# Kernel optimization log

Measured on AMD Instinct MI355X. Metric: run time of the kernel, lower is better.

The kernel has to match this reference:

```python
import jax, jax.numpy as jnp
import numpy as np

D_MODEL = 1024
N_HEADS = 16
N_KV_HEADS = 4
HEAD_DIM = D_MODEL // N_HEADS  # 64
N_REP = N_HEADS // N_KV_HEADS  # 4
THETA = 10000.0
LOGIT_CAP = 30.0
EPS = 1e-6
SCALE = HEAD_DIM ** -0.5


def rmsnorm(x, w):
    return x * jax.lax.rsqrt(jnp.mean(x * x, axis=-1, keepdims=True) + EPS) * w


def rope_tables(seq_len, dtype):
    inv_freq = 1.0 / (THETA ** (jnp.arange(0, HEAD_DIM, 2, dtype=jnp.float32) / HEAD_DIM))
    t = jnp.arange(seq_len, dtype=jnp.float32)
    freqs = jnp.outer(t, inv_freq)                      # [S, hd/2]
    emb = jnp.concatenate([freqs, freqs], axis=-1)      # [S, hd]
    return jnp.cos(emb).astype(dtype), jnp.sin(emb).astype(dtype)


def rotate_half(x):
    x1, x2 = jnp.split(x, 2, axis=-1)
    return jnp.concatenate([-x2, x1], axis=-1)


def apply_rope(x, cos, sin):
    # x: [B, H, S, hd]; cos/sin: [S, hd] broadcast over (B, H)
    return x * cos + rotate_half(x) * sin


def setup_inputs() -> dict:
    key = jax.random.key(0)
    ks = jax.random.split(key, 7)
    B, S = 4, 2048
    w = 0.02
    return {
        "x": jax.random.normal(ks[0], (B, S, D_MODEL), dtype=jnp.float32),
        "Wq": jax.random.normal(ks[1], (N_HEADS * HEAD_DIM, D_MODEL), dtype=jnp.float32) * w,
        "Wk": jax.random.normal(ks[2], (N_KV_HEADS * HEAD_DIM, D_MODEL), dtype=jnp.float32) * w,
        "Wv": jax.random.normal(ks[3], (N_KV_HEADS * HEAD_DIM, D_MODEL), dtype=jnp.float32) * w,
        "Wo": jax.random.normal(ks[4], (D_MODEL, N_HEADS * HEAD_DIM), dtype=jnp.float32) * w,
        "q_norm_w": jnp.ones((HEAD_DIM,), dtype=jnp.float32),
        "k_norm_w": jnp.ones((HEAD_DIM,), dtype=jnp.float32),
    }


def reference(x, Wq, Wk, Wv, Wo, q_norm_w, k_norm_w):
    B, S, _ = x.shape
    # projections (nn.Linear: y = x @ W^T)
    q = (x @ Wq.T).reshape(B, S, N_HEADS, HEAD_DIM).transpose(0, 2, 1, 3)      # [B,H,S,d]
    k = (x @ Wk.T).reshape(B, S, N_KV_HEADS, HEAD_DIM).transpose(0, 2, 1, 3)   # [B,Hkv,S,d]
    v = (x @ Wv.T).reshape(B, S, N_KV_HEADS, HEAD_DIM).transpose(0, 2, 1, 3)
    # QK-RMSNorm
    q = rmsnorm(q, q_norm_w)
    k = rmsnorm(k, k_norm_w)
    # RoPE
    cos, sin = rope_tables(S, x.dtype)
    q = apply_rope(q, cos, sin)
    k = apply_rope(k, cos, sin)
    # GQA expand (repeat_interleave over head dim)
    k_exp = jnp.repeat(k, N_REP, axis=1)  # [B,H,S,d]
    v_exp = jnp.repeat(v, N_REP, axis=1)
    # soft-capped attention (training path)
    scores = jnp.einsum('bhqd,bhkd->bhqk', q, k_exp) * SCALE
    scores = LOGIT_CAP * jnp.tanh(scores / LOGIT_CAP)
    causal = jnp.triu(jnp.ones((S, S), dtype=bool), k=1)  # kv_len - seq_len + 1 = 1
    scores = jnp.where(causal, -jnp.inf, scores)
    attn = jax.nn.softmax(scores, axis=-1)
    out = jnp.einsum('bhqk,bhkd->bhqd', attn, v_exp)
    out = out.transpose(0, 2, 1, 3).reshape(B, S, N_HEADS * HEAD_DIM)
    return out @ Wo.T
```

## Files before the change

### kernel.cpp

```cpp
#include <hip/hip_runtime.h>
#include <hip/hip_bf16.h>
#include <math.h>
#include <stdint.h>

#define D_MODEL 1024
#define NHEADS  16
#define NKV     4
#define HD      64
#define SEQ     2048
#define BATCH   4
#define MTOK    (BATCH*SEQ)
#define NQKV    (D_MODEL + 2*NKV*HD)
#define ASCALE  0.125f
#define CAP     30.0f

using f32x4  = __attribute__((ext_vector_type(4))) float;
using f32x2  = __attribute__((ext_vector_type(2))) float;
using bf16x8 = __attribute__((ext_vector_type(8))) short;

__device__ __forceinline__ unsigned short f2bf(float f) {
  union { float f; unsigned u; } v; v.f = f;
  unsigned u = v.u + 0x7fffu + ((v.u >> 16) & 1u);
  return (unsigned short)(u >> 16);
}
__device__ __forceinline__ unsigned short f2bf_hup(float f) {
  union { float f; unsigned u; } v; v.f = f;
  return (unsigned short)((v.u + 0x8000u) >> 16);
}
__device__ __forceinline__ float fexp2(float x) {
  return __builtin_amdgcn_exp2f(x);
}
__device__ __forceinline__ void async_copy16(void* lds, const void* g) {
  __builtin_amdgcn_global_load_lds(
      (const __attribute__((address_space(1))) unsigned int*)(uintptr_t)g,
      (__attribute__((address_space(3))) unsigned int*)(uintptr_t)lds, 16, 0, 0);
}

__global__ __launch_bounds__(256) void cvt_all(
    const float* __restrict__ x, const float* __restrict__ wq,
    const float* __restrict__ wk, const float* __restrict__ wv,
    const float* __restrict__ wo,
    unsigned short* __restrict__ xb, unsigned short* __restrict__ wqkv,
    unsigned short* __restrict__ wob) {
  const long i = (long)(blockIdx.x * 256 + threadIdx.x) * 4;
  const float* src; unsigned short* dst; long off;
  if (i < 8388608L)      { src = x;  dst = xb;             off = i; }
  else if (i < 9437184L) { src = wq; dst = wqkv;           off = i - 8388608L; }
  else if (i < 9699328L) { src = wk; dst = wqkv + 1048576; off = i - 9437184L; }
  else if (i < 9961472L) { src = wv; dst = wqkv + 1310720; off = i - 9699328L; }
  else                   { src = wo; dst = wob;            off = i - 9961472L; }
  float4 v = *(const float4*)(src + off);
  ushort4 o; o.x = f2bf(v.x); o.y = f2bf(v.y); o.z = f2bf(v.z); o.w = f2bf(v.w);
  *(ushort4*)(dst + off) = o;
}

__global__ __launch_bounds__(256) void gemm_qkv(
    const unsigned short* __restrict__ A, const unsigned short* __restrict__ B,
    const float* __restrict__ qw, const float* __restrict__ kw,
    unsigned short* __restrict__ Qn, unsigned short* __restrict__ Kn,
    unsigned short* __restrict__ Vt) {
  __shared__ __align__(16) unsigned short As[128 * 32];
  __shared__ __align__(16) unsigned short Bs[128 * 32];
  const int t = threadIdx.x;
  const int w = t >> 6, l = t & 63;
  const int mb = blockIdx.x, nb = blockIdx.y;
  const int wm = w & 1, wn = w >> 1;
  const int quad = l >> 4, ln = l & 15;
  const int K = D_MODEL;
  f32x4 acc[4][4] = {};
  const unsigned short* Ag = A + (size_t)(mb * 128 + w * 32) * K;
  const unsigned short* Bg = B + (size_t)(nb * 128 + w * 32) * K;
  char* Asw = (char*)As + w * 2048;
  char* Bsw = (char*)Bs + w * 2048;
  const int lrow = l >> 2, lcol = (l & 3) * 8;

  for (int kb = 0; kb < K; kb += 32) {
    async_copy16(Asw + l * 16,        Ag + (size_t)lrow * K + kb + lcol);
    async_copy16(Asw + 1024 + l * 16, Ag + (size_t)(16 + lrow) * K + kb + lcol);
    async_copy16(Bsw + l * 16,        Bg + (size_t)lrow * K + kb + lcol);
    async_copy16(Bsw + 1024 + l * 16, Bg + (size_t)(16 + lrow) * K + kb + lcol);
    __syncthreads();
    bf16x8 af[4], bfr[4];
#pragma unroll
    for (int mt = 0; mt < 4; ++mt)
      af[mt] = *(const bf16x8*)(As + (wm * 64 + mt * 16 + ln) * 32 + quad * 8);
#pragma unroll
    for (int nt = 0; nt < 4; ++nt)
      bfr[nt] = *(const bf16x8*)(Bs + (wn * 64 + nt * 16 + ln) * 32 + quad * 8);
#pragma unroll
    for (int mt = 0; mt < 4; ++mt)
#pragma unroll
      for (int nt = 0; nt < 4; ++nt)
        acc[mt][nt] = __builtin_amdgcn_mfma_f32_16x16x32_bf16(af[mt], bfr[nt], acc[mt][nt], 0, 0, 0);
    __syncthreads();
  }

  const int hs = nb * 2 + wn;
  const int bB = mb >> 4;
  const int sBase = ((mb & 15) * 128) + wm * 64;

  if (hs < 20) {
    const float* wgt = (hs < 16) ? qw : kw;
    float wv_[4];
#pragma unroll
    for (int nt = 0; nt < 4; ++nt) wv_[nt] = wgt[nt * 16 + ln];
    const float f0 = __expf(-(float)ln * 0.2878231366f);
    const float f1 = f0 * 0.01f;
    unsigned short* dst = (hs < 16)
        ? Qn + (size_t)(bB * 16 + hs) * SEQ * 64
        : Kn + (size_t)(bB * 4 + (hs - 16)) * SEQ * 64;
#pragma unroll
    for (int mt = 0; mt < 4; ++mt) {
#pragma unroll
      for (int r = 0; r < 4; ++r) {
        const int sTok = sBase + mt * 16 + quad * 4 + r;
        float ss = 0.f;
#pragma unroll
        for (int nt = 0; nt < 4; ++nt) ss = fmaf(acc[mt][nt][r], acc[mt][nt][r], ss);
        ss += __shfl_xor(ss, 1, 64); ss += __shfl_xor(ss, 2, 64);
        ss += __shfl_xor(ss, 4, 64); ss += __shfl_xor(ss, 8, 64);
        const float inv = rsqrtf(ss * (1.0f / 64.0f) + 1e-6f);
        float xn[4];
#pragma unroll
        for (int nt = 0; nt < 4; ++nt) xn[nt] = acc[mt][nt][r] * inv * wv_[nt];
        float sn0, cs0, sn1, cs1;
        __sincosf((float)sTok * f0, &sn0, &cs0);
        __sincosf((float)sTok * f1, &sn1, &cs1);
        const float o0 = xn[0] * cs0 - xn[2] * sn0;
        const float o1 = xn[1] * cs1 - xn[3] * sn1;
        const float o2 = xn[2] * cs0 + xn[0] * sn0;
        const float o3 = xn[3] * cs1 + xn[1] * sn1;
        const size_t ro = (size_t)sTok * 64 + ln;
        dst[ro]      = f2bf(o0);
        dst[ro + 16] = f2bf(o1);
        dst[ro + 32] = f2bf(o2);
        dst[ro + 48] = f2bf(o3);
      }
    }
  } else {
    unsigned short* dst = Vt + (size_t)(bB * 4 + (hs - 20)) * 64 * SEQ;
#pragma unroll
    for (int mt = 0; mt < 4; ++mt)
#pragma unroll
      for (int nt = 0; nt < 4; ++nt)
#pragma unroll
        for (int r = 0; r < 4; ++r) {
          const int sTok = sBase + mt * 16 + quad * 4 + r;
          dst[(size_t)(nt * 16 + ln) * SEQ + sTok] = f2bf(acc[mt][nt][r]);
        }
  }
}

__global__ __launch_bounds__(256) void gemm_bt_f32(
    const unsigned short* __restrict__ A, const unsigned short* __restrict__ B,
    float* __restrict__ C, int M, int N, int K) {
  __shared__ __align__(16) unsigned short As[128 * 32];
  __shared__ __align__(16) unsigned short Bs[128 * 32];
  const int t = threadIdx.x;
  const int w = t >> 6, l = t & 63;
  const int mb = blockIdx.x, nb = blockIdx.y;
  const int wm = w & 1, wn = w >> 1;
  f32x4 acc[4][4] = {};
  const unsigned short* Ag = A + (size_t)(mb * 128 + w * 32) * K;
  const unsigned short* Bg = B + (size_t)(nb * 128 + w * 32) * K;
  char* Asw = (char*)As + w * 2048;
  char* Bsw = (char*)Bs + w * 2048;
  const int lrow = l >> 2, lcol = (l & 3) * 8;

  for (int kb = 0; kb < K; kb += 32) {
    async_copy16(Asw + l * 16,        Ag + (size_t)lrow * K + kb + lcol);
    async_copy16(Asw + 1024 + l * 16, Ag + (size_t)(16 + lrow) * K + kb + lcol);
    async_copy16(Bsw + l * 16,        Bg + (size_t)lrow * K + kb + lcol);
    async_copy16(Bsw + 1024 + l * 16, Bg + (size_t)(16 + lrow) * K + kb + lcol);
    __syncthreads();
    bf16x8 af[4], bfr[4];
#pragma unroll
    for (int mt = 0; mt < 4; ++mt)
      af[mt] = *(const bf16x8*)(As + (wm * 64 + mt * 16 + (l & 15)) * 32 + (l >> 4) * 8);
#pragma unroll
    for (int nt = 0; nt < 4; ++nt)
      bfr[nt] = *(const bf16x8*)(Bs + (wn * 64 + nt * 16 + (l & 15)) * 32 + (l >> 4) * 8);
#pragma unroll
    for (int mt = 0; mt < 4; ++mt)
#pragma unroll
      for (int nt = 0; nt < 4; ++nt)
        acc[mt][nt] = __builtin_amdgcn_mfma_f32_16x16x32_bf16(af[mt], bfr[nt], acc[mt][nt], 0, 0, 0);
    __syncthreads();
  }
  const int row0 = mb * 128 + wm * 64, col0 = nb * 128 + wn * 64;
#pragma unroll
  for (int mt = 0; mt < 4; ++mt)
#pragma unroll
    for (int nt = 0; nt < 4; ++nt)
#pragma unroll
      for (int r = 0; r < 4; ++r) {
        int row = row0 + mt * 16 + (l >> 4) * 4 + r;
        int col = col0 + nt * 16 + (l & 15);
        C[(size_t)row * N + col] = acc[mt][nt][r];
      }
}

__global__ __launch_bounds__(256, 4) void attn(
    const unsigned short* __restrict__ Qn, const unsigned short* __restrict__ Kn,
    const unsigned short* __restrict__ Vtg, unsigned short* __restrict__ O) {
  __shared__ __align__(16) unsigned short Ks[4096];
  __shared__ __align__(16) unsigned short Vs[4096];
  __shared__ __align__(16) unsigned short Ps[8192];
  const int t = threadIdx.x, w = t >> 6, l = t & 63;
  const int quad = l >> 4, ln = l & 15;
  const int bid = blockIdx.x;
  const int qt = 15 - (bid >> 6);
  const int bh = bid & 63;
  const int h = bh & 15, b = bh >> 4;
  const int q0 = qt * 128;
  const int wq0 = q0 + w * 32;
  const unsigned short* Qh = Qn + ((size_t)(b * 16 + h)) * SEQ * 64;
  const unsigned short* Kg = Kn + ((size_t)(b * 4 + (h >> 2))) * SEQ * 64;
  const unsigned short* Vg = Vtg + ((size_t)(b * 4 + (h >> 2))) * 64 * SEQ;
  const int lrow = l >> 2;
  const int lswz = (((l & 3) ^ ((lrow >> 1) & 3)) * 8);
  const int qsw = (quad ^ ((ln >> 1) & 3)) << 4;

  bf16x8 aq[2][2];
#pragma unroll
  for (int mt = 0; mt < 2; ++mt)
#pragma unroll
    for (int ks = 0; ks < 2; ++ks)
      aq[mt][ks] = *(const bf16x8*)(Qh + (size_t)(wq0 + mt * 16 + ln) * 64 + ks * 32 + quad * 8);
  f32x4 o_acc[2][4] = {};
  f32x2 lp[2][2] = {};

  const float Cc = 0.18033688011112042f;
  const float B1 = -5.787037037e-6f;
  const float M2 = 11.541560327f;

  const int jmax = 2 * qt + 2;
  for (int jj = 0; jj < jmax; ++jj) {
    const int kv0 = jj * 64;
    __syncthreads();
#pragma unroll
    for (int i = 0; i < 2; ++i) {
      int s = w * 2 + i;
      int snt = s >> 1, sks = s & 1;
      async_copy16((char*)Ks + s * 1024,
                   Kg + (size_t)(kv0 + snt * 16 + lrow) * 64 + sks * 32 + lswz);
      async_copy16((char*)Vs + s * 1024,
                   Vg + (size_t)(snt * 16 + lrow) * SEQ + kv0 + sks * 32 + lswz);
    }
    __syncthreads();
    if (kv0 > wq0 + 31) continue;

    f32x4 sacc[2][4] = {};
    __builtin_amdgcn_s_setprio(1);
#pragma unroll
    for (int nt = 0; nt < 4; ++nt)
#pragma unroll
      for (int ks = 0; ks < 2; ++ks) {
        bf16x8 bk = *(const bf16x8*)((char*)Ks + (nt * 2 + ks) * 1024 + ln * 64 + qsw);
        sacc[0][nt] = __builtin_amdgcn_mfma_f32_16x16x32_bf16(aq[0][ks], bk, sacc[0][nt], 0, 0, 0);
        sacc[1][nt] = __builtin_amdgcn_mfma_f32_16x16x32_bf16(aq[1][ks], bk, sacc[1][nt], 0, 0, 0);
      }
    __builtin_amdgcn_s_setprio(0);

    const bool needMask = (kv0 + 63 > wq0);
#pragma unroll
    for (int mt = 0; mt < 2; ++mt)
#pragma unroll
      for (int nt = 0; nt < 4; ++nt) {
        const int col = nt * 16 + ln;
        const int base = w * 2048 + mt * 1024 + (col >> 5) * 512 +
                         ((((col >> 3) & 3) ^ quad) << 3) + (col & 7);
#pragma unroll
        for (int rp = 0; rp < 2; ++rp) {
          f32x2 s = { sacc[mt][nt][rp * 2], sacc[mt][nt][rp * 2 + 1] };
          f32x2 s2 = s * s;
          f32x2 tt = s2 * B1 + 1.0f;
          f32x2 arg = (s * Cc) * tt - M2;
          float pr0 = fexp2(arg.x), pr1 = fexp2(arg.y);
          if (needMask) {
            const int qrow = wq0 + mt * 16 + quad * 4 + rp * 2;
            if ((kv0 + col) > qrow)     pr0 = 0.0f;
            if ((kv0 + col) > qrow + 1) pr1 = 0.0f;
          }
          lp[mt][rp] += (f32x2){pr0, pr1};
          Ps[base + (quad * 4 + rp * 2) * 32]     = f2bf_hup(pr0);
          Ps[base + (quad * 4 + rp * 2 + 1) * 32] = f2bf_hup(pr1);
        }
      }
    __builtin_amdgcn_s_waitcnt(0xc07f);

    bf16x8 ap[2][2];
#pragma unroll
    for (int mt = 0; mt < 2; ++mt)
#pragma unroll
      for (int ks = 0; ks < 2; ++ks)
        ap[mt][ks] = *(const bf16x8*)((char*)Ps + w * 4096 + mt * 2048 + ks * 1024 +
                                      ln * 64 + ((quad ^ (ln >> 2)) << 4));
    __builtin_amdgcn_s_setprio(1);
#pragma unroll
    for (int nt = 0; nt < 4; ++nt)
#pragma unroll
      for (int ks = 0; ks < 2; ++ks) {
        bf16x8 bv = *(const bf16x8*)((char*)Vs + (nt * 2 + ks) * 1024 + ln * 64 + qsw);
        o_acc[0][nt] = __builtin_amdgcn_mfma_f32_16x16x32_bf16(ap[0][ks], bv, o_acc[0][nt], 0, 0, 0);
        o_acc[1][nt] = __builtin_amdgcn_mfma_f32_16x16x32_bf16(ap[1][ks], bv, o_acc[1][nt], 0, 0, 0);
      }
    __builtin_amdgcn_s_setprio(0);
  }

  float invl[2][4];
#pragma unroll
  for (int mt = 0; mt < 2; ++mt)
#pragma unroll
    for (int r = 0; r < 4; ++r) {
      float s = lp[mt][r >> 1][r & 1];
      s += __shfl_xor(s, 1, 64); s += __shfl_xor(s, 2, 64);
      s += __shfl_xor(s, 4, 64); s += __shfl_xor(s, 8, 64);
      invl[mt][r] = __builtin_amdgcn_rcpf(s);
    }
#pragma unroll
  for (int mt = 0; mt < 2; ++mt)
#pragma unroll
    for (int nt = 0; nt < 4; ++nt)
#pragma unroll
      for (int r = 0; r < 4; ++r) {
        int qrow = wq0 + mt * 16 + quad * 4 + r;
        int col = h * 64 + nt * 16 + ln;
        O[((size_t)(b * SEQ + qrow)) * 1024 + col] = f2bf_hup(o_acc[mt][nt][r] * invl[mt][r]);
      }
}

extern "C" void kernel_launch(void* const* d_in, const int* in_sizes, int n_in,
                              void* d_out, int out_size, void* d_ws, size_t ws_size,
                              hipStream_t stream) {
  const float* x  = (const float*)d_in[0];
  const float* Wq = (const float*)d_in[1];
  const float* Wk = (const float*)d_in[2];
  const float* Wv = (const float*)d_in[3];
  const float* Wo = (const float*)d_in[4];
  const float* qw = (const float*)d_in[5];
  const float* kw = (const float*)d_in[6];
  float* out = (float*)d_out;

  char* ws = (char*)d_ws;
  unsigned short* xb   = (unsigned short*)(ws);
  unsigned short* wqkv = (unsigned short*)(ws + 16777216);
  unsigned short* wo   = (unsigned short*)(ws + 19922944);
  unsigned short* Qn   = (unsigned short*)(ws + 22020096);
  unsigned short* Kn   = (unsigned short*)(ws + 38797312);
  unsigned short* Vtg  = (unsigned short*)(ws + 42991616);
  unsigned short* Ob   = (unsigned short*)(ws + 47185920);

  cvt_all<<<10752, 256, 0, stream>>>(x, Wq, Wk, Wv, Wo, xb, wqkv, wo);
  gemm_qkv<<<dim3(MTOK / 128, NQKV / 128), 256, 0, stream>>>(xb, wqkv, qw, kw, Qn, Kn, Vtg);
  attn<<<1024, 256, 0, stream>>>(Qn, Kn, Vtg, Ob);
  gemm_bt_f32<<<dim3(MTOK / 128, 1024 / 128), 256, 0, stream>>>(Ob, wo, out, MTOK, 1024, 1024);
}
```

Baseline: 238.5 us.

## Keep attention probabilities in registers via transposed QK^T and permlane swaps

Computes S^T by swapping the MFMA operands so that each lane holds the scores for one query row. The probabilities are then packed with v_cvt_pk_bf16_f32 and rearranged into the PV A-operand layout with permlane16/32 swaps, which removes the Ps shared-memory round trip, its LDS buffer and the wait. The row-sum reduction changes to match the new layout. LDS use and the store/load latency per tile go down, in exchange for cross-lane permute instructions and a new layout that must be correct.

```diff
diff --git a/kernel.cpp b/kernel.cpp
--- a/kernel.cpp
+++ b/kernel.cpp
@@ -17,6 +17,7 @@
 using f32x4  = __attribute__((ext_vector_type(4))) float;
 using f32x2  = __attribute__((ext_vector_type(2))) float;
 using bf16x8 = __attribute__((ext_vector_type(8))) short;
+using u32x4  = __attribute__((ext_vector_type(4))) unsigned int;
 
 __device__ __forceinline__ unsigned short f2bf(float f) {
   union { float f; unsigned u; } v; v.f = f;
@@ -205,7 +206,6 @@
     const unsigned short* __restrict__ Vtg, unsigned short* __restrict__ O) {
   __shared__ __align__(16) unsigned short Ks[4096];
   __shared__ __align__(16) unsigned short Vs[4096];
-  __shared__ __align__(16) unsigned short Ps[8192];
   const int t = threadIdx.x, w = t >> 6, l = t & 63;
   const int quad = l >> 4, ln = l & 15;
   const int bid = blockIdx.x;
@@ -228,11 +228,12 @@
     for (int ks = 0; ks < 2; ++ks)
       aq[mt][ks] = *(const bf16x8*)(Qh + (size_t)(wq0 + mt * 16 + ln) * 64 + ks * 32 + quad * 8);
   f32x4 o_acc[2][4] = {};
-  f32x2 lp[2][2] = {};
+  f32x2 lp[2] = {};
 
   const float Cc = 0.18033688011112042f;
   const float B1 = -5.787037037e-6f;
   const float M2 = 11.541560327f;
+  const int qr0 = wq0 + ln;
 
   const int jmax = 2 * qt + 2;
   for (int jj = 0; jj < jmax; ++jj) {
@@ -250,52 +251,57 @@
     __syncthreads();
     if (kv0 > wq0 + 31) continue;
 
-    f32x4 sacc[2][4] = {};
+    f32x4 st[4][2] = {};
     __builtin_amdgcn_s_setprio(1);
 #pragma unroll
     for (int nt = 0; nt < 4; ++nt)
 #pragma unroll
       for (int ks = 0; ks < 2; ++ks) {
         bf16x8 bk = *(const bf16x8*)((char*)Ks + (nt * 2 + ks) * 1024 + ln * 64 + qsw);
-        sacc[0][nt] = __builtin_amdgcn_mfma_f32_16x16x32_bf16(aq[0][ks], bk, sacc[0][nt], 0, 0, 0);
-        sacc[1][nt] = __builtin_amdgcn_mfma_f32_16x16x32_bf16(aq[1][ks], bk, sacc[1][nt], 0, 0, 0);
+        st[nt][0] = __builtin_amdgcn_mfma_f32_16x16x32_bf16(bk, aq[0][ks], st[nt][0], 0, 0, 0);
+        st[nt][1] = __builtin_amdgcn_mfma_f32_16x16x32_bf16(bk, aq[1][ks], st[nt][1], 0, 0, 0);
       }
     __builtin_amdgcn_s_setprio(0);
 
     const bool needMask = (kv0 + 63 > wq0);
-#pragma unroll
-    for (int mt = 0; mt < 2; ++mt)
-#pragma unroll
-      for (int nt = 0; nt < 4; ++nt) {
-        const int col = nt * 16 + ln;
-        const int base = w * 2048 + mt * 1024 + (col >> 5) * 512 +
-                         ((((col >> 3) & 3) ^ quad) << 3) + (col & 7);
+    bf16x8 ap[2][2];
+#pragma unroll
+    for (int mt = 0; mt < 2; ++mt) {
+      const int qrow = qr0 + mt * 16;
+      unsigned Wp[4][2];
+#pragma unroll
+      for (int nt = 0; nt < 4; ++nt)
 #pragma unroll
         for (int rp = 0; rp < 2; ++rp) {
-          f32x2 s = { sacc[mt][nt][rp * 2], sacc[mt][nt][rp * 2 + 1] };
+          f32x2 s = { st[nt][mt][rp * 2], st[nt][mt][rp * 2 + 1] };
           f32x2 s2 = s * s;
           f32x2 tt = s2 * B1 + 1.0f;
           f32x2 arg = (s * Cc) * tt - M2;
           float pr0 = fexp2(arg.x), pr1 = fexp2(arg.y);
           if (needMask) {
-            const int qrow = wq0 + mt * 16 + quad * 4 + rp * 2;
-            if ((kv0 + col) > qrow)     pr0 = 0.0f;
-            if ((kv0 + col) > qrow + 1) pr1 = 0.0f;
+            const int kvb = kv0 + nt * 16 + quad * 4 + rp * 2;
+            if (kvb > qrow)     pr0 = 0.0f;
+            if (kvb + 1 > qrow) pr1 = 0.0f;
           }
-          lp[mt][rp] += (f32x2){pr0, pr1};
-          Ps[base + (quad * 4 + rp * 2) * 32]     = f2bf_hup(pr0);
-          Ps[base + (quad * 4 + rp * 2 + 1) * 32] = f2bf_hup(pr1);
+          lp[mt] += (f32x2){pr0, pr1};
+          unsigned wpk;
+          asm("v_cvt_pk_bf16_f32 %0, %1, %2" : "=v"(wpk) : "v"(pr0), "v"(pr1));
+          Wp[nt][rp] = wpk;
         }
-      }
-    __builtin_amdgcn_s_waitcnt(0xc07f);
-
-    bf16x8 ap[2][2];
-#pragma unroll
-    for (int mt = 0; mt < 2; ++mt)
-#pragma unroll
-      for (int ks = 0; ks < 2; ++ks)
-        ap[mt][ks] = *(const bf16x8*)((char*)Ps + w * 4096 + mt * 2048 + ks * 1024 +
-                                      ln * 64 + ((quad ^ (ln >> 2)) << 4));
+#pragma unroll
+      for (int ks = 0; ks < 2; ++ks) {
+        unsigned a0 = Wp[2 * ks][0], b0 = Wp[2 * ks + 1][0];
+        unsigned a1 = Wp[2 * ks][1], b1 = Wp[2 * ks + 1][1];
+        asm("v_permlane32_swap_b32 %0, %1" : "+v"(a0), "+v"(b0));
+        asm("v_permlane16_swap_b32 %0, %1" : "+v"(a0), "+v"(b0));
+        asm("v_permlane32_swap_b32 %0, %1" : "+v"(a1), "+v"(b1));
+        asm("v_permlane16_swap_b32 %0, %1" : "+v"(a1), "+v"(b1));
+        union { u32x4 u; bf16x8 bv; } cc;
+        cc.u = (u32x4){a0, a1, b0, b1};
+        ap[mt][ks] = cc.bv;
+      }
+    }
+
     __builtin_amdgcn_s_setprio(1);
 #pragma unroll
     for (int nt = 0; nt < 4; ++nt)
@@ -310,14 +316,14 @@
 
   float invl[2][4];
 #pragma unroll
-  for (int mt = 0; mt < 2; ++mt)
-#pragma unroll
-    for (int r = 0; r < 4; ++r) {
-      float s = lp[mt][r >> 1][r & 1];
-      s += __shfl_xor(s, 1, 64); s += __shfl_xor(s, 2, 64);
-      s += __shfl_xor(s, 4, 64); s += __shfl_xor(s, 8, 64);
-      invl[mt][r] = __builtin_amdgcn_rcpf(s);
-    }
+  for (int mt = 0; mt < 2; ++mt) {
+    float s = lp[mt].x + lp[mt].y;
+    s += __shfl_xor(s, 16, 64);
+    s += __shfl_xor(s, 32, 64);
+#pragma unroll
+    for (int r = 0; r < 4; ++r)
+      invl[mt][r] = __builtin_amdgcn_rcpf(__shfl(s, quad * 4 + r, 64));
+  }
 #pragma unroll
   for (int mt = 0; mt < 2; ++mt)
 #pragma unroll
```

Measured after the change: 231.9 us. -2.7%, faster.
